# Performance work log

Measured on AMD Instinct MI355X. Metric: run time of the kernel, lower is better.

Reference implementation:

```python
import jax, jax.numpy as jnp
import numpy as np

N_HEAD = 16
ROPE_BASE = 10000.0


def setup_inputs() -> dict:
    key = jax.random.key(0)
    k1, k2, k3 = jax.random.split(key, 3)
    B, T, C = 2, 2048, 2048
    x = jax.random.normal(k1, (B, T, C), dtype=jnp.float32)
    # 0.02 init scale keeps attention logits in a sane range
    w_qkv = jax.random.normal(k2, (3 * C, C), dtype=jnp.float32) * 0.02
    w_proj = jax.random.normal(k3, (C, C), dtype=jnp.float32) * 0.02
    return {"x": x, "w_qkv": w_qkv, "w_proj": w_proj}


def _apply_rope(t, cos, sin):
    # t: [B, T, H, hd]; cos/sin: [T, hd//2]
    B, T, H, hd = t.shape
    ts = t.reshape(B, T, H, hd // 2, 2)
    x0, x1 = ts[..., 0], ts[..., 1]
    c = cos[None, :, None, :]
    s = sin[None, :, None, :]
    out = jnp.stack([x0 * c - x1 * s, x1 * c + x0 * s], axis=-1)
    return out.reshape(B, T, H, hd)


def reference(x, w_qkv, w_proj):
    B, T, C = x.shape
    H = N_HEAD
    hd = C // H

    qkv = x @ w_qkv.T                       # [B, T, 3C]
    q, k, v = jnp.split(qkv, 3, axis=2)
    q = q.reshape(B, T, H, hd)
    k = k.reshape(B, T, H, hd)              # present kv: pre-RoPE k, [B,T,H,hd]
    v = v.reshape(B, T, H, hd).transpose(0, 2, 1, 3)  # [B,H,T,hd]

    # RoPE cache (positions = arange(T) since past_key_value is None)
    theta = 1.0 / (ROPE_BASE ** (jnp.arange(0, hd, 2, dtype=jnp.float32) / hd))
    ang = jnp.arange(T, dtype=jnp.float32)[:, None] * theta[None, :]  # [T, hd//2]
    cos, sin = jnp.cos(ang), jnp.sin(ang)

    qr = _apply_rope(q, cos, sin).transpose(0, 2, 1, 3)  # [B,H,T,hd]
    kr = _apply_rope(k, cos, sin).transpose(0, 2, 1, 3)  # [B,H,T,hd]

    scale = 1.0 / jnp.sqrt(jnp.asarray(hd, dtype=qr.dtype))
    scores = jnp.einsum('bhqd,bhkd->bhqk', qr, kr) * scale  # [B,H,T,T]
    attn = jax.nn.softmax(scores, axis=-1)
    o = jnp.einsum('bhqk,bhkd->bhqd', attn, v)              # [B,H,T,hd]
    y = o.transpose(0, 2, 1, 3).reshape(B, T, C) @ w_proj.T
    return (y, k, v)
```

## Files before the change

### kernel.cpp

```cpp
#include <hip/hip_runtime.h>
#include <math.h>


typedef __bf16 bf16_t;
typedef __bf16 bf16x8 __attribute__((ext_vector_type(8)));
typedef __bf16 bf16x4v __attribute__((ext_vector_type(4)));
typedef float  f32x4  __attribute__((ext_vector_type(4)));

#define B_  2
#define T_  2048
#define C_  2048
#define SLICE_ ((size_t)B_ * T_ * C_)

__device__ __forceinline__ void glds16(const void* g, void* l) {
  __builtin_amdgcn_global_load_lds(
      (__attribute__((address_space(1))) void*)(void*)(const_cast<void*>(g)),
      (__attribute__((address_space(3))) void*)(l), 16, 0, 0);
}

__global__ __launch_bounds__(256) void k_prep(
    const float4* __restrict__ x, const float4* __restrict__ wqkv,
    const float4* __restrict__ wproj, bf16x4v* __restrict__ xb,
    bf16x4v* __restrict__ wqkvb, bf16x4v* __restrict__ wprojb,
    float2* __restrict__ tab) {
  int i = blockIdx.x * 256 + threadIdx.x;
  if (i < 2097152) {
    float4 v = x[i];
    bf16x4v o;
    o[0] = (bf16_t)v.x; o[1] = (bf16_t)v.y; o[2] = (bf16_t)v.z; o[3] = (bf16_t)v.w;
    xb[i] = o;
  } else if (i < 5242880) {
    int j = i - 2097152;
    float4 v = wqkv[j];
    bf16x4v o;
    o[0] = (bf16_t)v.x; o[1] = (bf16_t)v.y; o[2] = (bf16_t)v.z; o[3] = (bf16_t)v.w;
    wqkvb[j] = o;
  } else if (i < 6291456) {
    int j = i - 5242880;
    float4 v = wproj[j];
    bf16x4v o;
    o[0] = (bf16_t)v.x; o[1] = (bf16_t)v.y; o[2] = (bf16_t)v.z; o[3] = (bf16_t)v.w;
    wprojb[j] = o;
  } else {
    int j = i - 6291456;
    int t = j >> 6, jj = j & 63;
    float thf = (float)pow(10000.0, -(double)(2 * jj) / 128.0);
    float angf = (float)t * thf;
    double a = (double)angf;
    tab[j] = make_float2((float)cos(a), (float)sin(a));
  }
}

__global__ __launch_bounds__(256, 2) void k_qkv(
    const bf16_t* __restrict__ X, const bf16_t* __restrict__ W,
    const float2* __restrict__ tab,
    bf16_t* __restrict__ qb, bf16_t* __restrict__ kb, bf16_t* __restrict__ vtb,
    float* __restrict__ kout, float* __restrict__ vout) {
  const int K = 2048;
  __shared__ alignas(16) bf16_t smem[17408];
  bf16_t* As = smem;
  bf16_t* Bs = smem + 8192;
  const int tid = threadIdx.x;
  const int lane = tid & 63, wv = tid >> 6;
  const int wm = wv >> 1, wn = wv & 1;
  const int q4 = lane >> 4, l16 = lane & 15;
  const int m0 = blockIdx.x * 128, n0 = blockIdx.y * 128;

  const bf16_t* Ab = X + (size_t)m0 * K;
  const bf16_t* Wb = W + (size_t)n0 * K;

  f32x4 zero4 = {0.f, 0.f, 0.f, 0.f};
  f32x4 acc[4][4];
#pragma unroll
  for (int i = 0; i < 4; ++i)
#pragma unroll
    for (int j = 0; j < 4; ++j) acc[i][j] = zero4;

  for (int k0 = 0; k0 < K; k0 += 64) {
    __syncthreads();
#pragma unroll
    for (int i = 0; i < 4; ++i) {
      int ci = i * 256 + tid;
      glds16(Ab + (size_t)(ci >> 3) * K + k0 + (((ci & 7) ^ ((ci >> 3) & 7)) << 3),
             &As[(i * 256 + wv * 64) * 8]);
    }
#pragma unroll
    for (int i = 0; i < 4; ++i) {
      int ci = i * 256 + tid;
      glds16(Wb + (size_t)(ci >> 3) * K + k0 + (((ci & 7) ^ ((ci >> 3) & 7)) << 3),
             &Bs[(i * 256 + wv * 64) * 8]);
    }
    __syncthreads();
#pragma unroll
    for (int kk = 0; kk < 2; ++kk) {
      bf16x8 afrag[4], bfrag[4];
#pragma unroll
      for (int mf = 0; mf < 4; ++mf)
        afrag[mf] = *(const bf16x8*)&As[(wm * 64 + mf * 16 + l16) * 64 +
                                        ((((kk << 2) | q4) ^ (l16 & 7)) << 3)];
#pragma unroll
      for (int nf = 0; nf < 4; ++nf)
        bfrag[nf] = *(const bf16x8*)&Bs[(wn * 64 + nf * 16 + l16) * 64 +
                                        ((((kk << 2) | q4) ^ (l16 & 7)) << 3)];
#pragma unroll
      for (int mf = 0; mf < 4; ++mf)
#pragma unroll
        for (int nf = 0; nf < 4; ++nf)
          acc[mf][nf] = __builtin_amdgcn_mfma_f32_16x16x32_bf16(
              afrag[mf], bfrag[nf], acc[mf][nf], 0, 0, 0);
    }
  }

  __syncthreads();
  const int sec = n0 >> 11;
  const int t0 = m0 & 2047, bb = m0 >> 11, h = (n0 & 2047) >> 7;

  if (sec < 2) {
#pragma unroll
    for (int mf = 0; mf < 4; ++mf)
#pragma unroll
      for (int nf = 0; nf < 4; ++nf)
#pragma unroll
        for (int r = 0; r < 4; ++r) {
          int ml = wm * 64 + mf * 16 + q4 * 4 + r;
          int d = wn * 64 + nf * 16 + l16;
          float val = acc[mf][nf][r];
          float partner = __shfl_xor(val, 1);
          float2 cs = tab[(t0 + ml) * 64 + (d >> 1)];
          float rv = (d & 1) ? (val * cs.x + partner * cs.y)
                             : (val * cs.x - partner * cs.y);
          if (sec == 0) rv *= 0.08838834764831845f;
          else kout[(size_t)(m0 + ml) * 2048 + h * 128 + d] = val;
          smem[ml * 136 + d] = (bf16_t)rv;
        }
    __syncthreads();
    bf16_t* dst = (sec == 0 ? qb : kb);
    size_t gbase = ((size_t)(bb * 16 + h) * 2048 + t0) * 128;
#pragma unroll
    for (int i = 0; i < 8; ++i) {
      int ci = i * 256 + tid, ml = ci >> 4, cc = (ci & 15) * 8;
      *(bf16x8*)(dst + gbase + (size_t)ml * 128 + cc) =
          *(const bf16x8*)&smem[ml * 136 + cc];
    }
  } else {
#pragma unroll
    for (int mf = 0; mf < 4; ++mf)
#pragma unroll
      for (int nf = 0; nf < 4; ++nf)
#pragma unroll
        for (int r = 0; r < 4; ++r) {
          int ml = wm * 64 + mf * 16 + q4 * 4 + r;
          int d = wn * 64 + nf * 16 + l16;
          float val = acc[mf][nf][r];
          vout[((size_t)(bb * 16 + h) * 2048 + t0 + ml) * 128 + d] = val;
          smem[d * 136 + ml] = (bf16_t)val;
        }
    __syncthreads();
#pragma unroll
    for (int i = 0; i < 8; ++i) {
      int ci = i * 256 + tid, dr = ci >> 4, cc = (ci & 15) * 8;
      *(bf16x8*)(vtb + ((size_t)((bb * 16 + h) * 128 + dr)) * 2048 + t0 + cc) =
          *(const bf16x8*)&smem[dr * 136 + cc];
    }
  }
}

__global__ __launch_bounds__(256, 2) void k_attn(
    const bf16_t* __restrict__ qb, const bf16_t* __restrict__ kb,
    const bf16_t* __restrict__ vtb, bf16_t* __restrict__ ob) {
  __shared__ alignas(16) bf16_t Ps[128 * 80];
  __shared__ alignas(16) bf16_t Ks[64 * 128];
  __shared__ alignas(16) bf16_t Vts[128 * 64];

  const int tid = threadIdx.x;
  const int lane = tid & 63, wv = tid >> 6;
  const int q4 = lane >> 4, l16 = lane & 15;
  const int bh = blockIdx.x >> 4;
  const int q0 = (blockIdx.x & 15) * 128;

  const bf16_t* Qg = qb + (size_t)bh * T_ * 128 + (size_t)q0 * 128;
  const bf16_t* Kg = kb + (size_t)bh * T_ * 128;
  const bf16_t* Vg = vtb + (size_t)bh * 128 * T_;

  bf16x8 qa[2][4];
#pragma unroll
  for (int mf = 0; mf < 2; ++mf)
#pragma unroll
    for (int kf = 0; kf < 4; ++kf)
      qa[mf][kf] = *(const bf16x8*)(Qg + (size_t)(wv * 32 + mf * 16 + l16) * 128 +
                                    kf * 32 + q4 * 8);

  f32x4 zero4 = {0.f, 0.f, 0.f, 0.f};
  float lrow[2][4];
  f32x4 oacc[2][8];
#pragma unroll
  for (int mf = 0; mf < 2; ++mf) {
#pragma unroll
    for (int r = 0; r < 4; ++r) lrow[mf][r] = 0.f;
#pragma unroll
    for (int nf = 0; nf < 8; ++nf) oacc[mf][nf] = zero4;
  }

  bf16x8 kst[4], vst[4];
#pragma unroll
  for (int i = 0; i < 4; ++i) {
    int ci = i * 256 + tid;
    kst[i] = *(const bf16x8*)(Kg + (size_t)(ci >> 4) * 128 +
                              (((ci & 15) ^ ((ci >> 4) & 7)) << 3));
    vst[i] = *(const bf16x8*)(Vg + (size_t)(ci >> 3) * T_ +
                              (((ci & 7) ^ ((ci >> 3) & 7)) << 3));
  }

  for (int key0 = 0; key0 < T_; key0 += 64) {
    __syncthreads();
#pragma unroll
    for (int i = 0; i < 4; ++i) {
      int ci = i * 256 + tid;
      *(bf16x8*)&Ks[ci * 8] = kst[i];
      *(bf16x8*)&Vts[ci * 8] = vst[i];
    }
    __syncthreads();

    if (key0 + 64 < T_) {
      const bf16_t* Kg2 = Kg + (size_t)(key0 + 64) * 128;
      const bf16_t* Vg2 = Vg + key0 + 64;
#pragma unroll
      for (int i = 0; i < 4; ++i) {
        int ci = i * 256 + tid;
        kst[i] = *(const bf16x8*)(Kg2 + (size_t)(ci >> 4) * 128 +
                                  (((ci & 15) ^ ((ci >> 4) & 7)) << 3));
        vst[i] = *(const bf16x8*)(Vg2 + (size_t)(ci >> 3) * T_ +
                                  (((ci & 7) ^ ((ci >> 3) & 7)) << 3));
      }
    }

    f32x4 sacc[2][4];
#pragma unroll
    for (int mf = 0; mf < 2; ++mf)
#pragma unroll
      for (int nf = 0; nf < 4; ++nf) sacc[mf][nf] = zero4;
#pragma unroll
    for (int kf = 0; kf < 4; ++kf) {
      bf16x8 bfrag[4];
#pragma unroll
      for (int nf = 0; nf < 4; ++nf)
        bfrag[nf] = *(const bf16x8*)&Ks[(nf * 16 + l16) * 128 +
                                        ((((kf << 2) | q4) ^ (l16 & 7)) << 3)];
#pragma unroll
      for (int mf = 0; mf < 2; ++mf)
#pragma unroll
        for (int nf = 0; nf < 4; ++nf)
          sacc[mf][nf] = __builtin_amdgcn_mfma_f32_16x16x32_bf16(
              qa[mf][kf], bfrag[nf], sacc[mf][nf], 0, 0, 0);
    }

#pragma unroll
    for (int mf = 0; mf < 2; ++mf) {
#pragma unroll
      for (int r = 0; r < 4; ++r) {
        float p0 = __expf(sacc[mf][0][r]);
        float p1 = __expf(sacc[mf][1][r]);
        float p2 = __expf(sacc[mf][2][r]);
        float p3 = __expf(sacc[mf][3][r]);
        int prow = wv * 32 + mf * 16 + q4 * 4 + r;
        Ps[prow * 80 + 0 + l16]  = (bf16_t)p0;
        Ps[prow * 80 + 16 + l16] = (bf16_t)p1;
        Ps[prow * 80 + 32 + l16] = (bf16_t)p2;
        Ps[prow * 80 + 48 + l16] = (bf16_t)p3;
        lrow[mf][r] += (p0 + p1) + (p2 + p3);
      }
    }

#pragma unroll
    for (int kf2 = 0; kf2 < 2; ++kf2) {
      bf16x8 pa[2], vb[8];
#pragma unroll
      for (int mf = 0; mf < 2; ++mf)
        pa[mf] = *(const bf16x8*)&Ps[(wv * 32 + mf * 16 + l16) * 80 +
                                     kf2 * 32 + q4 * 8];
#pragma unroll
      for (int nf = 0; nf < 8; ++nf)
        vb[nf] = *(const bf16x8*)&Vts[(nf * 16 + l16) * 64 +
                                      ((((kf2 << 2) | q4) ^ (l16 & 7)) << 3)];
#pragma unroll
      for (int mf = 0; mf < 2; ++mf)
#pragma unroll
        for (int nf = 0; nf < 8; ++nf)
          oacc[mf][nf] = __builtin_amdgcn_mfma_f32_16x16x32_bf16(
              pa[mf], vb[nf], oacc[mf][nf], 0, 0, 0);
    }
  }

  const int b = bh >> 4, h = bh & 15;
#pragma unroll
  for (int mf = 0; mf < 2; ++mf) {
#pragma unroll
    for (int r = 0; r < 4; ++r) {
      float l = lrow[mf][r];
      l += __shfl_xor(l, 1);
      l += __shfl_xor(l, 2);
      l += __shfl_xor(l, 4);
      l += __shfl_xor(l, 8);
      float inv = 1.f / l;
      int t = q0 + wv * 32 + mf * 16 + q4 * 4 + r;
      size_t base = ((size_t)b * 2048 + t) * 2048 + h * 128;
#pragma unroll
      for (int nf = 0; nf < 8; ++nf)
        ob[base + nf * 16 + l16] = (bf16_t)(oacc[mf][nf][r] * inv);
    }
  }
}

__global__ __launch_bounds__(256, 2) void k_proj(
    const bf16_t* __restrict__ O, const bf16_t* __restrict__ Wp,
    float* __restrict__ Y) {
  const int K = 2048;
  __shared__ alignas(16) bf16_t As[128 * 64];
  __shared__ alignas(16) bf16_t Bs[128 * 64];
  const int tid = threadIdx.x;
  const int lane = tid & 63, wv = tid >> 6;
  const int wm = wv >> 1, wn = wv & 1;
  const int q4 = lane >> 4, l16 = lane & 15;
  const int m0 = blockIdx.x * 128, n0 = blockIdx.y * 128;

  const bf16_t* Ab = O + (size_t)m0 * K;
  const bf16_t* Wb = Wp + (size_t)n0 * K;

  f32x4 zero4 = {0.f, 0.f, 0.f, 0.f};
  f32x4 acc[4][4];
#pragma unroll
  for (int i = 0; i < 4; ++i)
#pragma unroll
    for (int j = 0; j < 4; ++j) acc[i][j] = zero4;

  for (int k0 = 0; k0 < K; k0 += 64) {
    __syncthreads();
#pragma unroll
    for (int i = 0; i < 4; ++i) {
      int ci = i * 256 + tid;
      glds16(Ab + (size_t)(ci >> 3) * K + k0 + (((ci & 7) ^ ((ci >> 3) & 7)) << 3),
             &As[(i * 256 + wv * 64) * 8]);
    }
#pragma unroll
    for (int i = 0; i < 4; ++i) {
      int ci = i * 256 + tid;
      glds16(Wb + (size_t)(ci >> 3) * K + k0 + (((ci & 7) ^ ((ci >> 3) & 7)) << 3),
             &Bs[(i * 256 + wv * 64) * 8]);
    }
    __syncthreads();
#pragma unroll
    for (int kk = 0; kk < 2; ++kk) {
      bf16x8 afrag[4], bfrag[4];
#pragma unroll
      for (int mf = 0; mf < 4; ++mf)
        afrag[mf] = *(const bf16x8*)&As[(wm * 64 + mf * 16 + l16) * 64 +
                                        ((((kk << 2) | q4) ^ (l16 & 7)) << 3)];
#pragma unroll
      for (int nf = 0; nf < 4; ++nf)
        bfrag[nf] = *(const bf16x8*)&Bs[(wn * 64 + nf * 16 + l16) * 64 +
                                        ((((kk << 2) | q4) ^ (l16 & 7)) << 3)];
#pragma unroll
      for (int mf = 0; mf < 4; ++mf)
#pragma unroll
        for (int nf = 0; nf < 4; ++nf)
          acc[mf][nf] = __builtin_amdgcn_mfma_f32_16x16x32_bf16(
              afrag[mf], bfrag[nf], acc[mf][nf], 0, 0, 0);
    }
  }
#pragma unroll
  for (int mf = 0; mf < 4; ++mf)
#pragma unroll
    for (int nf = 0; nf < 4; ++nf)
#pragma unroll
      for (int r = 0; r < 4; ++r) {
        int m = m0 + wm * 64 + mf * 16 + q4 * 4 + r;
        int n = n0 + wn * 64 + nf * 16 + l16;
        Y[(size_t)m * 2048 + n] = acc[mf][nf][r];
      }
}

extern "C" void kernel_launch(void* const* d_in, const int* in_sizes, int n_in,
                              void* d_out, int out_size, void* d_ws, size_t ws_size,
                              hipStream_t stream) {
  const float* x = (const float*)d_in[0];
  const float* wqkv = (const float*)d_in[1];
  const float* wproj = (const float*)d_in[2];

  float* y = (float*)d_out;
  float* kout = y + SLICE_;
  float* vout = y + 2 * SLICE_;

  char* w = (char*)d_ws;
  bf16_t* xb = (bf16_t*)w;      w += SLICE_ * 2;
  bf16_t* wqkvb = (bf16_t*)w;   w += (size_t)12582912 * 2;
  bf16_t* wprojb = (bf16_t*)w;  w += (size_t)4194304 * 2;
  bf16_t* qb = (bf16_t*)w;      w += SLICE_ * 2;
  bf16_t* kb = (bf16_t*)w;      w += SLICE_ * 2;
  bf16_t* vtb = (bf16_t*)w;     w += SLICE_ * 2;
  bf16_t* ob = (bf16_t*)w;      w += SLICE_ * 2;
  float2* tab = (float2*)w;     w += (size_t)131072 * 8;
  (void)ws_size; (void)in_sizes; (void)n_in; (void)out_size;

  k_prep<<<25088, 256, 0, stream>>>((const float4*)x, (const float4*)wqkv,
                                    (const float4*)wproj, (bf16x4v*)xb,
                                    (bf16x4v*)wqkvb, (bf16x4v*)wprojb, tab);

  dim3 gq(32, 48);
  k_qkv<<<gq, 256, 0, stream>>>(xb, wqkvb, tab, qb, kb, vtb, kout, vout);
  k_attn<<<512, 256, 0, stream>>>(qb, kb, vtb, ob);
  dim3 gp(32, 16);
  k_proj<<<gp, 256, 0, stream>>>(ob, wprojb, y);
}
```

Measured before the change: 387.1 us.

## Double-buffer K/V tiles in attention, use 512-thread blocks and exp2 softmax

The attention kernel now uses 512-thread blocks covering 256 queries each, and keeps two LDS buffers for K and V tiles. This cuts each loop iteration to a single barrier and lets the next tile load overlap with compute. The log2(e) factor is folded into the Q scaling so softmax can call exp2f instead of __expf. The grid drops to 256 blocks with 104 KB of dynamic LDS and one block per CU, which may leave some of the mi355x's CUs idle or reduce latency hiding.

```diff
diff --git a/kernel.cpp b/kernel.cpp
--- a/kernel.cpp
+++ b/kernel.cpp
@@ -129,7 +129,7 @@
           float2 cs = tab[(t0 + ml) * 64 + (d >> 1)];
           float rv = (d & 1) ? (val * cs.x + partner * cs.y)
                              : (val * cs.x - partner * cs.y);
-          if (sec == 0) rv *= 0.08838834764831845f;
+          if (sec == 0) rv *= 0.08838834764831845f * 1.4426950408889634f;
           else kout[(size_t)(m0 + ml) * 2048 + h * 128 + d] = val;
           smem[ml * 136 + d] = (bf16_t)rv;
         }
@@ -165,18 +165,46 @@
   }
 }
 
-__global__ __launch_bounds__(256, 2) void k_attn(
+__device__ __forceinline__ void attn_load(const bf16_t* __restrict__ Kg,
+                                          const bf16_t* __restrict__ Vg,
+                                          int key0, int tid, bf16x8 (&kst)[2],
+                                          bf16x8 (&vst)[2]) {
+#pragma unroll
+  for (int i = 0; i < 2; ++i) {
+    int ci = i * 512 + tid;
+    kst[i] = *(const bf16x8*)(Kg + (size_t)(key0 + (ci >> 4)) * 128 +
+                              (((ci & 15) ^ ((ci >> 4) & 7)) << 3));
+    vst[i] = *(const bf16x8*)(Vg + (size_t)(ci >> 3) * T_ + key0 +
+                              (((ci & 7) ^ ((ci >> 3) & 7)) << 3));
+  }
+}
+
+__device__ __forceinline__ void attn_write(bf16_t* Kd, bf16_t* Vd, int tid,
+                                           const bf16x8 (&kst)[2],
+                                           const bf16x8 (&vst)[2]) {
+#pragma unroll
+  for (int i = 0; i < 2; ++i) {
+    int ci = i * 512 + tid;
+    *(bf16x8*)&Kd[ci * 8] = kst[i];
+    *(bf16x8*)&Vd[ci * 8] = vst[i];
+  }
+}
+
+__global__ __launch_bounds__(512, 1) void k_attn(
     const bf16_t* __restrict__ qb, const bf16_t* __restrict__ kb,
     const bf16_t* __restrict__ vtb, bf16_t* __restrict__ ob) {
-  __shared__ alignas(16) bf16_t Ps[128 * 80];
-  __shared__ alignas(16) bf16_t Ks[64 * 128];
-  __shared__ alignas(16) bf16_t Vts[128 * 64];
+  extern __shared__ char asmem[];
+  bf16_t* Ps  = (bf16_t*)asmem;
+  bf16_t* Ks0 = (bf16_t*)(asmem + 40960);
+  bf16_t* Ks1 = (bf16_t*)(asmem + 57344);
+  bf16_t* Vt0 = (bf16_t*)(asmem + 73728);
+  bf16_t* Vt1 = (bf16_t*)(asmem + 90112);
 
   const int tid = threadIdx.x;
   const int lane = tid & 63, wv = tid >> 6;
   const int q4 = lane >> 4, l16 = lane & 15;
-  const int bh = blockIdx.x >> 4;
-  const int q0 = (blockIdx.x & 15) * 128;
+  const int bh = blockIdx.x >> 3;
+  const int q0 = (blockIdx.x & 7) * 256;
 
   const bf16_t* Qg = qb + (size_t)bh * T_ * 128 + (size_t)q0 * 128;
   const bf16_t* Kg = kb + (size_t)bh * T_ * 128;
@@ -201,37 +229,18 @@
     for (int nf = 0; nf < 8; ++nf) oacc[mf][nf] = zero4;
   }
 
-  bf16x8 kst[4], vst[4];
-#pragma unroll
-  for (int i = 0; i < 4; ++i) {
-    int ci = i * 256 + tid;
-    kst[i] = *(const bf16x8*)(Kg + (size_t)(ci >> 4) * 128 +
-                              (((ci & 15) ^ ((ci >> 4) & 7)) << 3));
-    vst[i] = *(const bf16x8*)(Vg + (size_t)(ci >> 3) * T_ +
-                              (((ci & 7) ^ ((ci >> 3) & 7)) << 3));
-  }
-
-  for (int key0 = 0; key0 < T_; key0 += 64) {
-    __syncthreads();
-#pragma unroll
-    for (int i = 0; i < 4; ++i) {
-      int ci = i * 256 + tid;
-      *(bf16x8*)&Ks[ci * 8] = kst[i];
-      *(bf16x8*)&Vts[ci * 8] = vst[i];
-    }
-    __syncthreads();
-
-    if (key0 + 64 < T_) {
-      const bf16_t* Kg2 = Kg + (size_t)(key0 + 64) * 128;
-      const bf16_t* Vg2 = Vg + key0 + 64;
-#pragma unroll
-      for (int i = 0; i < 4; ++i) {
-        int ci = i * 256 + tid;
-        kst[i] = *(const bf16x8*)(Kg2 + (size_t)(ci >> 4) * 128 +
-                                  (((ci & 15) ^ ((ci >> 4) & 7)) << 3));
-        vst[i] = *(const bf16x8*)(Vg2 + (size_t)(ci >> 3) * T_ +
-                                  (((ci & 7) ^ ((ci >> 3) & 7)) << 3));
-      }
+  bf16x8 kst[2], vst[2];
+  attn_load(Kg, Vg, 0, tid, kst, vst);
+  attn_write(Ks0, Vt0, tid, kst, vst);
+  attn_load(Kg, Vg, 64, tid, kst, vst);
+
+  for (int t = 0; t < 32; ++t) {
+    __syncthreads();
+    bf16_t* Ksc = (t & 1) ? Ks1 : Ks0;
+    bf16_t* Vtc = (t & 1) ? Vt1 : Vt0;
+    if (t < 31) {
+      attn_write((t & 1) ? Ks0 : Ks1, (t & 1) ? Vt0 : Vt1, tid, kst, vst);
+      if (t < 30) attn_load(Kg, Vg, (t + 2) * 64, tid, kst, vst);
     }
 
     f32x4 sacc[2][4];
@@ -244,8 +253,8 @@
       bf16x8 bfrag[4];
 #pragma unroll
       for (int nf = 0; nf < 4; ++nf)
-        bfrag[nf] = *(const bf16x8*)&Ks[(nf * 16 + l16) * 128 +
-                                        ((((kf << 2) | q4) ^ (l16 & 7)) << 3)];
+        bfrag[nf] = *(const bf16x8*)&Ksc[(nf * 16 + l16) * 128 +
+                                         ((((kf << 2) | q4) ^ (l16 & 7)) << 3)];
 #pragma unroll
       for (int mf = 0; mf < 2; ++mf)
 #pragma unroll
@@ -258,10 +267,10 @@
     for (int mf = 0; mf < 2; ++mf) {
 #pragma unroll
       for (int r = 0; r < 4; ++r) {
-        float p0 = __expf(sacc[mf][0][r]);
-        float p1 = __expf(sacc[mf][1][r]);
-        float p2 = __expf(sacc[mf][2][r]);
-        float p3 = __expf(sacc[mf][3][r]);
+        float p0 = exp2f(sacc[mf][0][r]);
+        float p1 = exp2f(sacc[mf][1][r]);
+        float p2 = exp2f(sacc[mf][2][r]);
+        float p3 = exp2f(sacc[mf][3][r]);
         int prow = wv * 32 + mf * 16 + q4 * 4 + r;
         Ps[prow * 80 + 0 + l16]  = (bf16_t)p0;
         Ps[prow * 80 + 16 + l16] = (bf16_t)p1;
@@ -280,7 +289,7 @@
                                      kf2 * 32 + q4 * 8];
 #pragma unroll
       for (int nf = 0; nf < 8; ++nf)
-        vb[nf] = *(const bf16x8*)&Vts[(nf * 16 + l16) * 64 +
+        vb[nf] = *(const bf16x8*)&Vtc[(nf * 16 + l16) * 64 +
                                       ((((kf2 << 2) | q4) ^ (l16 & 7)) << 3)];
 #pragma unroll
       for (int mf = 0; mf < 2; ++mf)
@@ -401,13 +410,20 @@
   float2* tab = (float2*)w;     w += (size_t)131072 * 8;
   (void)ws_size; (void)in_sizes; (void)n_in; (void)out_size;
 
+  static int smem_set = 0;
+  if (!smem_set) {
+    hipFuncSetAttribute((const void*)k_attn,
+                        hipFuncAttributeMaxDynamicSharedMemorySize, 106496);
+    smem_set = 1;
+  }
+
   k_prep<<<25088, 256, 0, stream>>>((const float4*)x, (const float4*)wqkv,
                                     (const float4*)wproj, (bf16x4v*)xb,
                                     (bf16x4v*)wqkvb, (bf16x4v*)wprojb, tab);
 
   dim3 gq(32, 48);
   k_qkv<<<gq, 256, 0, stream>>>(xb, wqkvb, tab, qb, kb, vtb, kout, vout);
-  k_attn<<<512, 256, 0, stream>>>(qb, kb, vtb, ob);
+  k_attn<<<256, 512, 106496, stream>>>(qb, kb, vtb, ob);
   dim3 gp(32, 16);
   k_proj<<<gp, 256, 0, stream>>>(ob, wprojb, y);
 }
```

Result: no change. 390.9 us (+1.0%).
